# Kernel tuning notes

Hardware: AMD Instinct MI355X
Metric: run time of the kernel (lower is better)

The kernel has to match this reference:

```python
import jax, jax.numpy as jnp
import numpy as np

E = 32      # num_experts
K = 4       # num_experts_per_tok
C = 1280


def setup_inputs() -> dict:
    key = jax.random.key(0)
    k0, k1, k2, k3, k4 = jax.random.split(key, 5)
    B, S, D, I = 4, 2048, 1024, 512
    return {
        "hidden_states": jax.random.normal(k0, (B, S, D), jnp.float32),
        "router_w": jax.random.normal(k1, (E, D), jnp.float32) * 0.02,   # nn.Linear(hidden, E).weight
        "gate_w": jax.random.normal(k2, (E, I, D), jnp.float32) * 0.02,
        "up_w": jax.random.normal(k3, (E, I, D), jnp.float32) * 0.02,
        "down_w": jax.random.normal(k4, (E, D, I), jnp.float32) * 0.02,
    }


def reference(hidden_states, router_w, gate_w, up_w, down_w):
    B, S, D = hidden_states.shape
    x = hidden_states.reshape(-1, D)                       # [T, D]
    T = x.shape[0]

    # Router: softmax in fp32, top-k, renormalize (norm_topk_prob=True)
    router_logits = x @ router_w.T                          # [T, E]
    probs = jax.nn.softmax(router_logits.astype(jnp.float32), axis=-1)
    w, sel = jax.lax.top_k(probs, K)                        # [T, K]
    w = w / jnp.sum(w, axis=-1, keepdims=True)
    w = w.astype(x.dtype)

    # Flatten (token, slot) dispatch rows
    e_flat = sel.reshape(-1)                                # [T*K]
    tok = jnp.repeat(jnp.arange(T), K)                      # [T*K]

    # Position of each row within its expert's buffer
    oh = jax.nn.one_hot(e_flat, E, dtype=jnp.int32)         # [T*K, E]
    pos = jnp.take_along_axis(jnp.cumsum(oh, axis=0), e_flat[:, None], axis=1)[:, 0] - 1
    valid = pos < C

    # Dispatch: scatter tokens into [E, C, D]; overflow rows go to slot C and are dropped
    pos_w = jnp.minimum(pos, C)
    buf = jnp.zeros((E, C + 1, D), x.dtype).at[e_flat, pos_w].set(x[tok])[:, :C]

    # Per-expert SwiGLU MLP as grouped matmuls
    g = jnp.einsum('ecd,eid->eci', buf, gate_w)
    u = jnp.einsum('ecd,eid->eci', buf, up_w)
    h = jax.nn.silu(g) * u
    y = jnp.einsum('eci,edi->ecd', h, down_w)               # [E, C, D]

    # Combine: gather expert outputs back and scatter-add into tokens
    pos_r = jnp.minimum(pos, C - 1)
    gathered = y[e_flat, pos_r]                             # [T*K, D]
    coef = w.reshape(-1) * valid.astype(x.dtype)
    final = jax.ops.segment_sum(gathered * coef[:, None], tok, num_segments=T)

    return final.reshape(B, S, D), router_logits
```

## Files before the change

### kernel.cpp

```cpp
#include <hip/hip_runtime.h>

#define T_TOK 8192
#define D_DIM 1024
#define E_NUM 32
#define K_TOP 4
#define CAP 1280
#define I_DIM 512

#define BM 128
#define BN 128
#define BK 32

typedef float f32x4 __attribute__((ext_vector_type(4)));
typedef short s16x8 __attribute__((ext_vector_type(8)));

static __device__ __forceinline__ unsigned short f2bf(float f) {
    unsigned int u = __float_as_uint(f);
    unsigned int r = (u + 0x7fffu + ((u >> 16) & 1u)) >> 16;
    return (unsigned short)r;
}
static __device__ __forceinline__ float bf2f(unsigned short s) {
    return __uint_as_float(((unsigned int)s) << 16);
}

static __device__ __forceinline__ void gload16(const unsigned short* g, unsigned short* l) {
    __builtin_amdgcn_global_load_lds(
        (const __attribute__((address_space(1))) unsigned int*)g,
        (__attribute__((address_space(3))) unsigned int*)l,
        16, 0, 0);
}

#define GW_F4 4194304L
__global__ __launch_bounds__(256) void cvt_kernel(
    const float* __restrict__ gw,
    const float* __restrict__ uw, const float* __restrict__ dw,
    unsigned short* __restrict__ gbf,
    unsigned short* __restrict__ ubf, unsigned short* __restrict__ dbf) {
    long i = (long)blockIdx.x * 256 + threadIdx.x;
    const float* src; unsigned short* dst; long off;
    if (i < GW_F4)        { src = gw; dst = gbf; off = i; }
    else if (i < 2*GW_F4) { src = uw; dst = ubf; off = i - GW_F4; }
    else                  { src = dw; dst = dbf; off = i - 2*GW_F4; }
    float4 v = ((const float4*)src)[off];
    ushort4 b;
    b.x = f2bf(v.x); b.y = f2bf(v.y); b.z = f2bf(v.z); b.w = f2bf(v.w);
    ((ushort4*)dst)[off] = b;
}

__global__ __launch_bounds__(256) void router_kernel(
    const float* __restrict__ x, const float* __restrict__ rw,
    float* __restrict__ logits, unsigned short* __restrict__ xbf) {
    int t = (blockIdx.x * 256 + threadIdx.x) >> 6;
    int lane = threadIdx.x & 63;
    const float* xr = x + (size_t)t * D_DIM;
    float xf[16];
#pragma unroll
    for (int j = 0; j < 16; ++j) xf[j] = xr[lane + 64 * j];
    unsigned short* xb = xbf + (size_t)t * D_DIM;
#pragma unroll
    for (int j = 0; j < 16; ++j) xb[lane + 64 * j] = f2bf(xf[j]);
#pragma unroll 1
    for (int e = 0; e < E_NUM; ++e) {
        const float* wr = rw + (size_t)e * D_DIM;
        float acc = 0.f;
#pragma unroll
        for (int j = 0; j < 16; ++j) acc = fmaf(xf[j], wr[lane + 64 * j], acc);
#pragma unroll
        for (int off = 32; off; off >>= 1) acc += __shfl_xor(acc, off);
        if (lane == 0) logits[(size_t)t * E_NUM + e] = acc;
    }
}

__global__ __launch_bounds__(256) void topk_kernel(
    const float* __restrict__ logits,
    int* __restrict__ counts, int* __restrict__ rowtok,
    int* __restrict__ tokslot, float* __restrict__ tokcoef) {
    __shared__ float lg[256 * 33];
    __shared__ int hist[E_NUM];
    __shared__ int base[E_NUM];
    int tid = threadIdx.x;
    int t0 = blockIdx.x * 256;
    if (tid < E_NUM) hist[tid] = 0;
#pragma unroll
    for (int i = 0; i < E_NUM; ++i) {
        int idx = i * 256 + tid;
        lg[(idx >> 5) * 33 + (idx & 31)] = logits[(size_t)t0 * E_NUM + idx];
    }
    __syncthreads();

    float p[E_NUM];
    float m = -1e30f;
#pragma unroll
    for (int e = 0; e < E_NUM; ++e) { p[e] = lg[tid * 33 + e]; m = fmaxf(m, p[e]); }
#pragma unroll
    for (int e = 0; e < E_NUM; ++e) p[e] = __expf(p[e] - m);

    float wv[K_TOP]; int sel[K_TOP];
#pragma unroll
    for (int k = 0; k < K_TOP; ++k) {
        float best = -1.0f; int bi = 0;
#pragma unroll
        for (int e = 0; e < E_NUM; ++e) if (p[e] > best) { best = p[e]; bi = e; }
        wv[k] = best; sel[k] = bi; p[bi] = -2.0f;
    }

    int lofs[K_TOP];
#pragma unroll
    for (int k = 0; k < K_TOP; ++k) lofs[k] = atomicAdd(&hist[sel[k]], 1);
    __syncthreads();
    if (tid < E_NUM) base[tid] = atomicAdd(&counts[tid], hist[tid]);
    __syncthreads();

    float inv = 1.0f / (wv[0] + wv[1] + wv[2] + wv[3]);
    int t = t0 + tid;
#pragma unroll
    for (int k = 0; k < K_TOP; ++k) {
        int e = sel[k];
        int slot = base[e] + lofs[k];
        if (slot < CAP) {
            rowtok[e * CAP + slot] = t;
            tokslot[t * K_TOP + k] = e * CAP + slot;
        } else {
            tokslot[t * K_TOP + k] = -1;
        }
        tokcoef[t * K_TOP + k] = wv[k] * inv;
    }
}

__global__ __launch_bounds__(256) void gateup_kernel(
    const unsigned short* __restrict__ xbf,
    const unsigned short* __restrict__ gbf, const unsigned short* __restrict__ ubf,
    const int* __restrict__ counts, const int* __restrict__ rowtok,
    unsigned short* __restrict__ h_ws) {
    int bid = blockIdx.x;
    int xcd = bid & 7;
    int slot = bid >> 3;
    int e = xcd + 8 * (slot / 40);
    int r = slot % 40;
    int mt = r >> 2;
    int nt = r & 3;
    int n_e = counts[e]; if (n_e > CAP) n_e = CAP;
    if (mt * BM >= n_e) return;

    __shared__ unsigned short As[2][BM * BK];
    __shared__ unsigned short Bg[2][BM * BK];
    __shared__ unsigned short Bu[2][BM * BK];
    __shared__ int toks[BM];

    int tid = threadIdx.x, lane = tid & 63, wv = tid >> 6;
    if (tid < BM) {
        int rr = mt * BM + tid;
        toks[tid] = (rr < n_e) ? rowtok[e * CAP + rr] : rowtok[e * CAP];
    }
    __syncthreads();

    int rA0 = (wv * 2 + 0) * 16 + (lane >> 2);
    int rA1 = rA0 + 16;
    int cst = (lane & 3) * 8;
    const unsigned short* gaA0 = xbf + (size_t)toks[rA0] * D_DIM + cst;
    const unsigned short* gaA1 = xbf + (size_t)toks[rA1] * D_DIM + cst;
    const unsigned short* gaG0 = gbf + ((size_t)e * I_DIM + nt * BN + rA0) * D_DIM + cst;
    const unsigned short* gaG1 = gbf + ((size_t)e * I_DIM + nt * BN + rA1) * D_DIM + cst;
    const unsigned short* gaU0 = ubf + ((size_t)e * I_DIM + nt * BN + rA0) * D_DIM + cst;
    const unsigned short* gaU1 = ubf + ((size_t)e * I_DIM + nt * BN + rA1) * D_DIM + cst;
    int l0 = (wv * 2 + 0) * 512;
    int l1 = (wv * 2 + 1) * 512;

    int wm = (wv >> 1) * 64;
    int wn = (wv & 1) * 64;

    f32x4 accg[4][4] = {};
    f32x4 accu[4][4] = {};

    gload16(gaA0, &As[0][l0]); gload16(gaA1, &As[0][l1]);
    gload16(gaG0, &Bg[0][l0]); gload16(gaG1, &Bg[0][l1]);
    gload16(gaU0, &Bu[0][l0]); gload16(gaU1, &Bu[0][l1]);

    for (int kk = 0; kk < D_DIM; kk += BK) {
        int p = (kk >> 5) & 1;
        __syncthreads();

        if (kk + BK < D_DIM) {
            int q = p ^ 1, k2 = kk + BK;
            gload16(gaA0 + k2, &As[q][l0]); gload16(gaA1 + k2, &As[q][l1]);
            gload16(gaG0 + k2, &Bg[q][l0]); gload16(gaG1 + k2, &Bg[q][l1]);
            gload16(gaU0 + k2, &Bu[q][l0]); gload16(gaU1 + k2, &Bu[q][l1]);
        }

        s16x8 af[4], bgf[4], buf[4];
#pragma unroll
        for (int mi = 0; mi < 4; ++mi)
            af[mi] = *(const s16x8*)&As[p][(wm + mi * 16 + (lane & 15)) * BK + (lane >> 4) * 8];
#pragma unroll
        for (int ni = 0; ni < 4; ++ni) {
            bgf[ni] = *(const s16x8*)&Bg[p][(wn + ni * 16 + (lane & 15)) * BK + (lane >> 4) * 8];
            buf[ni] = *(const s16x8*)&Bu[p][(wn + ni * 16 + (lane & 15)) * BK + (lane >> 4) * 8];
        }
#pragma unroll
        for (int mi = 0; mi < 4; ++mi)
#pragma unroll
            for (int ni = 0; ni < 4; ++ni) {
                accg[mi][ni] = __builtin_amdgcn_mfma_f32_16x16x32_bf16(af[mi], bgf[ni], accg[mi][ni], 0, 0, 0);
                accu[mi][ni] = __builtin_amdgcn_mfma_f32_16x16x32_bf16(af[mi], buf[ni], accu[mi][ni], 0, 0, 0);
            }
    }

    int rq = (lane >> 4) * 4;
    int cq = lane & 15;
#pragma unroll
    for (int mi = 0; mi < 4; ++mi)
#pragma unroll
        for (int ni = 0; ni < 4; ++ni)
#pragma unroll
            for (int rr = 0; rr < 4; ++rr) {
                int grow = mt * BM + wm + mi * 16 + rq + rr;
                if (grow < n_e) {
                    float g = accg[mi][ni][rr];
                    float hv = g / (1.0f + __expf(-g)) * accu[mi][ni][rr];
                    int icol = nt * BN + wn + ni * 16 + cq;
                    h_ws[((size_t)e * CAP + grow) * I_DIM + icol] = f2bf(hv);
                }
            }
}

__global__ __launch_bounds__(256) void down_kernel(
    const unsigned short* __restrict__ h_ws, const unsigned short* __restrict__ dbf,
    const int* __restrict__ counts, unsigned short* __restrict__ y_ws) {
    int bid = blockIdx.x;
    int xcd = bid & 7;
    int slot = bid >> 3;
    int e = xcd + 8 * (slot / 80);
    int r = slot % 80;
    int mt = r >> 3;
    int nt = r & 7;
    int n_e = counts[e]; if (n_e > CAP) n_e = CAP;
    if (mt * BM >= n_e) return;

    __shared__ unsigned short As[2][BM * BK];
    __shared__ unsigned short Bd[2][BM * BK];

    int tid = threadIdx.x, lane = tid & 63, wv = tid >> 6;

    int rA0 = (wv * 2 + 0) * 16 + (lane >> 2);
    int rA1 = rA0 + 16;
    int cst = (lane & 3) * 8;
    const unsigned short* gaA0 = h_ws + ((size_t)e * CAP + mt * BM + rA0) * I_DIM + cst;
    const unsigned short* gaA1 = h_ws + ((size_t)e * CAP + mt * BM + rA1) * I_DIM + cst;
    const unsigned short* gaB0 = dbf + ((size_t)e * D_DIM + nt * BN + rA0) * I_DIM + cst;
    const unsigned short* gaB1 = dbf + ((size_t)e * D_DIM + nt * BN + rA1) * I_DIM + cst;
    int l0 = (wv * 2 + 0) * 512;
    int l1 = (wv * 2 + 1) * 512;

    int wm = (wv >> 1) * 64;
    int wn = (wv & 1) * 64;

    f32x4 acc[4][4] = {};

    gload16(gaA0, &As[0][l0]); gload16(gaA1, &As[0][l1]);
    gload16(gaB0, &Bd[0][l0]); gload16(gaB1, &Bd[0][l1]);

    for (int kk = 0; kk < I_DIM; kk += BK) {
        int p = (kk >> 5) & 1;
        __syncthreads();

        if (kk + BK < I_DIM) {
            int q = p ^ 1, k2 = kk + BK;
            gload16(gaA0 + k2, &As[q][l0]); gload16(gaA1 + k2, &As[q][l1]);
            gload16(gaB0 + k2, &Bd[q][l0]); gload16(gaB1 + k2, &Bd[q][l1]);
        }

        s16x8 af[4], bf[4];
#pragma unroll
        for (int mi = 0; mi < 4; ++mi)
            af[mi] = *(const s16x8*)&As[p][(wm + mi * 16 + (lane & 15)) * BK + (lane >> 4) * 8];
#pragma unroll
        for (int ni = 0; ni < 4; ++ni)
            bf[ni] = *(const s16x8*)&Bd[p][(wn + ni * 16 + (lane & 15)) * BK + (lane >> 4) * 8];
#pragma unroll
        for (int mi = 0; mi < 4; ++mi)
#pragma unroll
            for (int ni = 0; ni < 4; ++ni)
                acc[mi][ni] = __builtin_amdgcn_mfma_f32_16x16x32_bf16(af[mi], bf[ni], acc[mi][ni], 0, 0, 0);
    }

    int rq = (lane >> 4) * 4;
    int cq = lane & 15;
#pragma unroll
    for (int mi = 0; mi < 4; ++mi)
#pragma unroll
        for (int ni = 0; ni < 4; ++ni)
#pragma unroll
            for (int rr = 0; rr < 4; ++rr) {
                int grow = mt * BM + wm + mi * 16 + rq + rr;
                if (grow < n_e) {
                    int dcol = nt * BN + wn + ni * 16 + cq;
                    y_ws[((size_t)e * CAP + grow) * D_DIM + dcol] = f2bf(acc[mi][ni][rr]);
                }
            }
}

__global__ __launch_bounds__(256) void combine_kernel(
    const unsigned short* __restrict__ y_ws,
    const int* __restrict__ tokslot, const float* __restrict__ tokcoef,
    float* __restrict__ out) {
    int t = (blockIdx.x * 256 + threadIdx.x) >> 6;
    int lane = threadIdx.x & 63;
    float acc[16] = {};
#pragma unroll
    for (int k = 0; k < K_TOP; ++k) {
        int slot = tokslot[t * K_TOP + k];
        if (slot >= 0) {
            float c = tokcoef[t * K_TOP + k];
            const unsigned short* row = y_ws + (size_t)slot * D_DIM + lane * 16;
            s16x8 v0 = *(const s16x8*)row;
            s16x8 v1 = *(const s16x8*)(row + 8);
#pragma unroll
            for (int j = 0; j < 8; ++j) acc[j]     = fmaf(c, bf2f((unsigned short)v0[j]), acc[j]);
#pragma unroll
            for (int j = 0; j < 8; ++j) acc[8 + j] = fmaf(c, bf2f((unsigned short)v1[j]), acc[8 + j]);
        }
    }
    float* o = out + (size_t)t * D_DIM + lane * 16;
#pragma unroll
    for (int j = 0; j < 4; ++j)
        ((float4*)o)[j] = make_float4(acc[4 * j], acc[4 * j + 1], acc[4 * j + 2], acc[4 * j + 3]);
}

extern "C" void kernel_launch(void* const* d_in, const int* in_sizes, int n_in,
                              void* d_out, int out_size, void* d_ws, size_t ws_size,
                              hipStream_t stream) {
    const float* x  = (const float*)d_in[0];
    const float* rw = (const float*)d_in[1];
    const float* gw = (const float*)d_in[2];
    const float* uw = (const float*)d_in[3];
    const float* dw = (const float*)d_in[4];
    float* out = (float*)d_out;
    float* logits = out + (size_t)T_TOK * D_DIM;

    char* ws = (char*)d_ws;
    size_t off = 0;
    unsigned short* xbf = (unsigned short*)(ws + off); off += (size_t)T_TOK * D_DIM * 2;
    unsigned short* gbf = (unsigned short*)(ws + off); off += (size_t)E_NUM * I_DIM * D_DIM * 2;
    unsigned short* ubf = (unsigned short*)(ws + off); off += (size_t)E_NUM * I_DIM * D_DIM * 2;
    unsigned short* y_ws = xbf;
    unsigned short* dbf = (unsigned short*)(ws + off); off += (size_t)E_NUM * D_DIM * I_DIM * 2;
    unsigned short* h_ws = (unsigned short*)(ws + off); off += (size_t)E_NUM * CAP * I_DIM * 2;
    int* counts = (int*)(ws + off); off += 256;
    int* rowtok = (int*)(ws + off); off += (size_t)E_NUM * CAP * 4;
    int* tokslot = (int*)(ws + off); off += (size_t)T_TOK * K_TOP * 4;
    float* tokcoef = (float*)(ws + off); off += (size_t)T_TOK * K_TOP * 4;

    hipMemsetAsync(counts, 0, E_NUM * 4, stream);

    cvt_kernel<<<(int)((3 * GW_F4) / 256), 256, 0, stream>>>(gw, uw, dw, gbf, ubf, dbf);
    router_kernel<<<T_TOK / 4, 256, 0, stream>>>(x, rw, logits, xbf);
    topk_kernel<<<T_TOK / 256, 256, 0, stream>>>(logits, counts, rowtok, tokslot, tokcoef);
    gateup_kernel<<<E_NUM * (CAP / BM) * (I_DIM / BN), 256, 0, stream>>>(xbf, gbf, ubf, counts, rowtok, h_ws);
    down_kernel<<<E_NUM * (CAP / BM) * (D_DIM / BN), 256, 0, stream>>>(h_ws, dbf, counts, y_ws);
    combine_kernel<<<T_TOK / 4, 256, 0, stream>>>(y_ws, tokslot, tokcoef, out);
}
```

Before: 533.5 us.

## Enlarge grouped-GEMM tiles to 256-row blocks with 512 threads and BK=64

Both expert GEMM kernels move to 512-thread blocks with larger tiles: gate/up uses 256x128 tiles and down uses 256x256 tiles, each with a 64-wide K step split into two MFMA sub-steps. The aim is more operand reuse per LDS load, fewer global loads of weights and gathered tokens, and half as many barrier iterations. The cost is much more LDS per block (up to 128KB in down_kernel), more accumulator registers, and coarser tiles, so more work is wasted on partially filled experts and fewer blocks can run at once.

Result: faster. 500.4 us (-6.2%).

```diff
diff --git a/kernel.cpp b/kernel.cpp
--- a/kernel.cpp
+++ b/kernel.cpp
@@ -6,10 +6,6 @@
 #define K_TOP 4
 #define CAP 1280
 #define I_DIM 512
-
-#define BM 128
-#define BN 128
-#define BK 32
 
 typedef float f32x4 __attribute__((ext_vector_type(4)));
 typedef short s16x8 __attribute__((ext_vector_type(8)));
@@ -127,7 +123,7 @@
     }
 }
 
-__global__ __launch_bounds__(256) void gateup_kernel(
+__global__ __launch_bounds__(512, 2) void gateup_kernel(
     const unsigned short* __restrict__ xbf,
     const unsigned short* __restrict__ gbf, const unsigned short* __restrict__ ubf,
     const int* __restrict__ counts, const int* __restrict__ rowtok,
@@ -135,74 +131,90 @@
     int bid = blockIdx.x;
     int xcd = bid & 7;
     int slot = bid >> 3;
-    int e = xcd + 8 * (slot / 40);
-    int r = slot % 40;
+    int e = xcd + 8 * (slot / 20);
+    int r = slot % 20;
     int mt = r >> 2;
     int nt = r & 3;
     int n_e = counts[e]; if (n_e > CAP) n_e = CAP;
-    if (mt * BM >= n_e) return;
-
-    __shared__ unsigned short As[2][BM * BK];
-    __shared__ unsigned short Bg[2][BM * BK];
-    __shared__ unsigned short Bu[2][BM * BK];
-    __shared__ int toks[BM];
+    if (mt * 256 >= n_e) return;
+
+    __shared__ unsigned short As[2][256 * 64];
+    __shared__ unsigned short Bg[2][128 * 64];
+    __shared__ unsigned short Bu[2][128 * 64];
+    __shared__ int toks[256];
 
     int tid = threadIdx.x, lane = tid & 63, wv = tid >> 6;
-    if (tid < BM) {
-        int rr = mt * BM + tid;
+    if (tid < 256) {
+        int rr = mt * 256 + tid;
         toks[tid] = (rr < n_e) ? rowtok[e * CAP + rr] : rowtok[e * CAP];
     }
     __syncthreads();
 
-    int rA0 = (wv * 2 + 0) * 16 + (lane >> 2);
-    int rA1 = rA0 + 16;
-    int cst = (lane & 3) * 8;
-    const unsigned short* gaA0 = xbf + (size_t)toks[rA0] * D_DIM + cst;
-    const unsigned short* gaA1 = xbf + (size_t)toks[rA1] * D_DIM + cst;
-    const unsigned short* gaG0 = gbf + ((size_t)e * I_DIM + nt * BN + rA0) * D_DIM + cst;
-    const unsigned short* gaG1 = gbf + ((size_t)e * I_DIM + nt * BN + rA1) * D_DIM + cst;
-    const unsigned short* gaU0 = ubf + ((size_t)e * I_DIM + nt * BN + rA0) * D_DIM + cst;
-    const unsigned short* gaU1 = ubf + ((size_t)e * I_DIM + nt * BN + rA1) * D_DIM + cst;
-    int l0 = (wv * 2 + 0) * 512;
-    int l1 = (wv * 2 + 1) * 512;
+    int row8 = tid >> 3;
+    int c8 = (tid & 7) * 8;
+    int ldst = tid * 8;
+    const unsigned short* aB[4];
+#pragma unroll
+    for (int j = 0; j < 4; ++j)
+        aB[j] = xbf + (size_t)toks[j * 64 + row8] * D_DIM + c8;
+    const unsigned short* gB[2];
+    const unsigned short* uB[2];
+#pragma unroll
+    for (int j = 0; j < 2; ++j) {
+        gB[j] = gbf + ((size_t)e * I_DIM + nt * 128 + j * 64 + row8) * D_DIM + c8;
+        uB[j] = ubf + ((size_t)e * I_DIM + nt * 128 + j * 64 + row8) * D_DIM + c8;
+    }
 
     int wm = (wv >> 1) * 64;
     int wn = (wv & 1) * 64;
+    int fr = lane & 15;
+    int fc = (lane >> 4) * 8;
 
     f32x4 accg[4][4] = {};
     f32x4 accu[4][4] = {};
 
-    gload16(gaA0, &As[0][l0]); gload16(gaA1, &As[0][l1]);
-    gload16(gaG0, &Bg[0][l0]); gload16(gaG1, &Bg[0][l1]);
-    gload16(gaU0, &Bu[0][l0]); gload16(gaU1, &Bu[0][l1]);
-
-    for (int kk = 0; kk < D_DIM; kk += BK) {
-        int p = (kk >> 5) & 1;
+#pragma unroll
+    for (int j = 0; j < 4; ++j) gload16(aB[j], &As[0][j * 4096 + ldst]);
+#pragma unroll
+    for (int j = 0; j < 2; ++j) {
+        gload16(gB[j], &Bg[0][j * 4096 + ldst]);
+        gload16(uB[j], &Bu[0][j * 4096 + ldst]);
+    }
+
+    for (int kb = 0; kb < D_DIM; kb += 64) {
+        int p = (kb >> 6) & 1;
         __syncthreads();
 
-        if (kk + BK < D_DIM) {
-            int q = p ^ 1, k2 = kk + BK;
-            gload16(gaA0 + k2, &As[q][l0]); gload16(gaA1 + k2, &As[q][l1]);
-            gload16(gaG0 + k2, &Bg[q][l0]); gload16(gaG1 + k2, &Bg[q][l1]);
-            gload16(gaU0 + k2, &Bu[q][l0]); gload16(gaU1 + k2, &Bu[q][l1]);
-        }
-
-        s16x8 af[4], bgf[4], buf[4];
-#pragma unroll
-        for (int mi = 0; mi < 4; ++mi)
-            af[mi] = *(const s16x8*)&As[p][(wm + mi * 16 + (lane & 15)) * BK + (lane >> 4) * 8];
-#pragma unroll
-        for (int ni = 0; ni < 4; ++ni) {
-            bgf[ni] = *(const s16x8*)&Bg[p][(wn + ni * 16 + (lane & 15)) * BK + (lane >> 4) * 8];
-            buf[ni] = *(const s16x8*)&Bu[p][(wn + ni * 16 + (lane & 15)) * BK + (lane >> 4) * 8];
-        }
-#pragma unroll
-        for (int mi = 0; mi < 4; ++mi)
+        if (kb + 64 < D_DIM) {
+            int q = p ^ 1, k2 = kb + 64;
+#pragma unroll
+            for (int j = 0; j < 4; ++j) gload16(aB[j] + k2, &As[q][j * 4096 + ldst]);
+#pragma unroll
+            for (int j = 0; j < 2; ++j) {
+                gload16(gB[j] + k2, &Bg[q][j * 4096 + ldst]);
+                gload16(uB[j] + k2, &Bu[q][j * 4096 + ldst]);
+            }
+        }
+
+#pragma unroll
+        for (int kk = 0; kk < 2; ++kk) {
+            s16x8 af[4], bgf[4], buf_[4];
+#pragma unroll
+            for (int mi = 0; mi < 4; ++mi)
+                af[mi] = *(const s16x8*)&As[p][(wm + mi * 16 + fr) * 64 + kk * 32 + fc];
 #pragma unroll
             for (int ni = 0; ni < 4; ++ni) {
-                accg[mi][ni] = __builtin_amdgcn_mfma_f32_16x16x32_bf16(af[mi], bgf[ni], accg[mi][ni], 0, 0, 0);
-                accu[mi][ni] = __builtin_amdgcn_mfma_f32_16x16x32_bf16(af[mi], buf[ni], accu[mi][ni], 0, 0, 0);
-            }
+                bgf[ni]  = *(const s16x8*)&Bg[p][(wn + ni * 16 + fr) * 64 + kk * 32 + fc];
+                buf_[ni] = *(const s16x8*)&Bu[p][(wn + ni * 16 + fr) * 64 + kk * 32 + fc];
+            }
+#pragma unroll
+            for (int mi = 0; mi < 4; ++mi)
+#pragma unroll
+                for (int ni = 0; ni < 4; ++ni) {
+                    accg[mi][ni] = __builtin_amdgcn_mfma_f32_16x16x32_bf16(af[mi], bgf[ni],  accg[mi][ni], 0, 0, 0);
+                    accu[mi][ni] = __builtin_amdgcn_mfma_f32_16x16x32_bf16(af[mi], buf_[ni], accu[mi][ni], 0, 0, 0);
+                }
+        }
     }
 
     int rq = (lane >> 4) * 4;
@@ -213,87 +225,99 @@
         for (int ni = 0; ni < 4; ++ni)
 #pragma unroll
             for (int rr = 0; rr < 4; ++rr) {
-                int grow = mt * BM + wm + mi * 16 + rq + rr;
+                int grow = mt * 256 + wm + mi * 16 + rq + rr;
                 if (grow < n_e) {
                     float g = accg[mi][ni][rr];
                     float hv = g / (1.0f + __expf(-g)) * accu[mi][ni][rr];
-                    int icol = nt * BN + wn + ni * 16 + cq;
+                    int icol = nt * 128 + wn + ni * 16 + cq;
                     h_ws[((size_t)e * CAP + grow) * I_DIM + icol] = f2bf(hv);
                 }
             }
 }
 
-__global__ __launch_bounds__(256) void down_kernel(
+__global__ __launch_bounds__(512, 2) void down_kernel(
     const unsigned short* __restrict__ h_ws, const unsigned short* __restrict__ dbf,
     const int* __restrict__ counts, unsigned short* __restrict__ y_ws) {
     int bid = blockIdx.x;
     int xcd = bid & 7;
     int slot = bid >> 3;
-    int e = xcd + 8 * (slot / 80);
-    int r = slot % 80;
-    int mt = r >> 3;
-    int nt = r & 7;
+    int e = xcd + 8 * (slot / 20);
+    int r = slot % 20;
+    int mt = r >> 2;
+    int nt = r & 3;
     int n_e = counts[e]; if (n_e > CAP) n_e = CAP;
-    if (mt * BM >= n_e) return;
-
-    __shared__ unsigned short As[2][BM * BK];
-    __shared__ unsigned short Bd[2][BM * BK];
+    if (mt * 256 >= n_e) return;
+
+    __shared__ unsigned short As[2][256 * 64];
+    __shared__ unsigned short Bd[2][256 * 64];
 
     int tid = threadIdx.x, lane = tid & 63, wv = tid >> 6;
 
-    int rA0 = (wv * 2 + 0) * 16 + (lane >> 2);
-    int rA1 = rA0 + 16;
-    int cst = (lane & 3) * 8;
-    const unsigned short* gaA0 = h_ws + ((size_t)e * CAP + mt * BM + rA0) * I_DIM + cst;
-    const unsigned short* gaA1 = h_ws + ((size_t)e * CAP + mt * BM + rA1) * I_DIM + cst;
-    const unsigned short* gaB0 = dbf + ((size_t)e * D_DIM + nt * BN + rA0) * I_DIM + cst;
-    const unsigned short* gaB1 = dbf + ((size_t)e * D_DIM + nt * BN + rA1) * I_DIM + cst;
-    int l0 = (wv * 2 + 0) * 512;
-    int l1 = (wv * 2 + 1) * 512;
-
-    int wm = (wv >> 1) * 64;
-    int wn = (wv & 1) * 64;
-
-    f32x4 acc[4][4] = {};
-
-    gload16(gaA0, &As[0][l0]); gload16(gaA1, &As[0][l1]);
-    gload16(gaB0, &Bd[0][l0]); gload16(gaB1, &Bd[0][l1]);
-
-    for (int kk = 0; kk < I_DIM; kk += BK) {
-        int p = (kk >> 5) & 1;
+    int row8 = tid >> 3;
+    int c8 = (tid & 7) * 8;
+    int ldst = tid * 8;
+    const unsigned short* aB[4];
+    const unsigned short* bB[4];
+#pragma unroll
+    for (int j = 0; j < 4; ++j) {
+        aB[j] = h_ws + ((size_t)e * CAP + mt * 256 + j * 64 + row8) * I_DIM + c8;
+        bB[j] = dbf  + ((size_t)e * D_DIM + nt * 256 + j * 64 + row8) * I_DIM + c8;
+    }
+
+    int wm = (wv >> 2) * 128;
+    int wn = (wv & 3) * 64;
+    int fr = lane & 15;
+    int fc = (lane >> 4) * 8;
+
+    f32x4 acc[8][4] = {};
+
+#pragma unroll
+    for (int j = 0; j < 4; ++j) {
+        gload16(aB[j], &As[0][j * 4096 + ldst]);
+        gload16(bB[j], &Bd[0][j * 4096 + ldst]);
+    }
+
+    for (int kb = 0; kb < I_DIM; kb += 64) {
+        int p = (kb >> 6) & 1;
         __syncthreads();
 
-        if (kk + BK < I_DIM) {
-            int q = p ^ 1, k2 = kk + BK;
-            gload16(gaA0 + k2, &As[q][l0]); gload16(gaA1 + k2, &As[q][l1]);
-            gload16(gaB0 + k2, &Bd[q][l0]); gload16(gaB1 + k2, &Bd[q][l1]);
-        }
-
-        s16x8 af[4], bf[4];
-#pragma unroll
-        for (int mi = 0; mi < 4; ++mi)
-            af[mi] = *(const s16x8*)&As[p][(wm + mi * 16 + (lane & 15)) * BK + (lane >> 4) * 8];
-#pragma unroll
-        for (int ni = 0; ni < 4; ++ni)
-            bf[ni] = *(const s16x8*)&Bd[p][(wn + ni * 16 + (lane & 15)) * BK + (lane >> 4) * 8];
-#pragma unroll
-        for (int mi = 0; mi < 4; ++mi)
+        if (kb + 64 < I_DIM) {
+            int q = p ^ 1, k2 = kb + 64;
+#pragma unroll
+            for (int j = 0; j < 4; ++j) {
+                gload16(aB[j] + k2, &As[q][j * 4096 + ldst]);
+                gload16(bB[j] + k2, &Bd[q][j * 4096 + ldst]);
+            }
+        }
+
+#pragma unroll
+        for (int kk = 0; kk < 2; ++kk) {
+            s16x8 af[8], bf[4];
+#pragma unroll
+            for (int mi = 0; mi < 8; ++mi)
+                af[mi] = *(const s16x8*)&As[p][(wm + mi * 16 + fr) * 64 + kk * 32 + fc];
 #pragma unroll
             for (int ni = 0; ni < 4; ++ni)
-                acc[mi][ni] = __builtin_amdgcn_mfma_f32_16x16x32_bf16(af[mi], bf[ni], acc[mi][ni], 0, 0, 0);
+                bf[ni] = *(const s16x8*)&Bd[p][(wn + ni * 16 + fr) * 64 + kk * 32 + fc];
+#pragma unroll
+            for (int mi = 0; mi < 8; ++mi)
+#pragma unroll
+                for (int ni = 0; ni < 4; ++ni)
+                    acc[mi][ni] = __builtin_amdgcn_mfma_f32_16x16x32_bf16(af[mi], bf[ni], acc[mi][ni], 0, 0, 0);
+        }
     }
 
     int rq = (lane >> 4) * 4;
     int cq = lane & 15;
 #pragma unroll
-    for (int mi = 0; mi < 4; ++mi)
+    for (int mi = 0; mi < 8; ++mi)
 #pragma unroll
         for (int ni = 0; ni < 4; ++ni)
 #pragma unroll
             for (int rr = 0; rr < 4; ++rr) {
-                int grow = mt * BM + wm + mi * 16 + rq + rr;
+                int grow = mt * 256 + wm + mi * 16 + rq + rr;
                 if (grow < n_e) {
-                    int dcol = nt * BN + wn + ni * 16 + cq;
+                    int dcol = nt * 256 + wn + ni * 16 + cq;
                     y_ws[((size_t)e * CAP + grow) * D_DIM + dcol] = f2bf(acc[mi][ni][rr]);
                 }
             }
@@ -355,7 +379,7 @@
     cvt_kernel<<<(int)((3 * GW_F4) / 256), 256, 0, stream>>>(gw, uw, dw, gbf, ubf, dbf);
     router_kernel<<<T_TOK / 4, 256, 0, stream>>>(x, rw, logits, xbf);
     topk_kernel<<<T_TOK / 256, 256, 0, stream>>>(logits, counts, rowtok, tokslot, tokcoef);
-    gateup_kernel<<<E_NUM * (CAP / BM) * (I_DIM / BN), 256, 0, stream>>>(xbf, gbf, ubf, counts, rowtok, h_ws);
-    down_kernel<<<E_NUM * (CAP / BM) * (D_DIM / BN), 256, 0, stream>>>(h_ws, dbf, counts, y_ws);
+    gateup_kernel<<<E_NUM * (CAP / 256) * (I_DIM / 128), 512, 0, stream>>>(xbf, gbf, ubf, counts, rowtok, h_ws);
+    down_kernel<<<E_NUM * (CAP / 256) * (D_DIM / 256), 512, 0, stream>>>(h_ws, dbf, counts, y_ws);
     combine_kernel<<<T_TOK / 4, 256, 0, stream>>>(y_ws, tokslot, tokcoef, out);
 }
```
